# Optimization experiments

Measured on AMD Instinct MI355X. Metric: run time of the kernel, lower is better.

Reference implementation:

```python
import jax, jax.numpy as jnp
import numpy as np

N_NODES = 20000
N_EDGES = 32000
BN_EPS = 1e-5


def _w(key, fan_in, fan_out):
    return jax.random.normal(key, (fan_in, fan_out), jnp.float32) / np.sqrt(fan_in).astype(np.float32)


def setup_inputs() -> dict:
    key = jax.random.key(0)
    ks = jax.random.split(key, 16)
    x = jax.random.normal(ks[0], (N_NODES, 5120), jnp.float32)
    edge_index = jax.random.randint(ks[1], (2, N_EDGES), 0, N_NODES, dtype=jnp.int64)
    return dict(
        x=x,
        W1l=_w(ks[2], 5120, 1680), b1=jnp.zeros((1680,), jnp.float32), W1r=_w(ks[3], 5120, 1680),
        W2l=_w(ks[4], 1680, 640), b2=jnp.zeros((640,), jnp.float32), W2r=_w(ks[5], 1680, 640),
        bn_gamma=jax.random.uniform(ks[6], (1680,), jnp.float32, 0.5, 1.5),
        bn_beta=jax.random.normal(ks[7], (1680,), jnp.float32) * 0.1,
        bn_mean=jnp.zeros((1680,), jnp.float32),
        bn_var=jnp.ones((1680,), jnp.float32),
        lin1_W=_w(ks[8], 640, 320), lin1_b=jnp.zeros((320,), jnp.float32),
        lin2_W=_w(ks[9], 320, 160), lin2_b=jnp.zeros((160,), jnp.float32),
        lin3_W=_w(ks[10], 160, 2), lin3_b=jnp.zeros((2,), jnp.float32),
        edge_index=edge_index,
    )


def _segment_mean(feat, dst, n):
    # mean-aggregate messages feat[e] into their destination node; 0 for isolated nodes (PyG semantics)
    s = jax.ops.segment_sum(feat, dst, num_segments=n)
    cnt = jax.ops.segment_sum(jnp.ones((dst.shape[0],), feat.dtype), dst, num_segments=n)
    return s / jnp.maximum(cnt, 1.0)[:, None]


def reference(x, W1l, b1, W1r, W2l, b2, W2r, bn_gamma, bn_beta, bn_mean, bn_var,
              lin1_W, lin1_b, lin2_W, lin2_b, lin3_W, lin3_b, edge_index):
    src, dst = edge_index[0], edge_index[1]
    n = x.shape[0]
    # SAGEConv 1: lin_l(mean_j x_j) + lin_r(x_i)
    h = _segment_mean(x[src], dst, n) @ W1l + b1 + x @ W1r
    h = jax.nn.relu(h)
    # BatchNorm1d in eval mode (running stats); dropout inactive in eval
    h = (h - bn_mean) * jax.lax.rsqrt(bn_var + BN_EPS) * bn_gamma + bn_beta
    # SAGEConv 2
    h2 = _segment_mean(h[src], dst, n) @ W2l + b2 + h @ W2r
    o = jax.nn.relu(h2)
    o = jax.nn.relu(o @ lin1_W + lin1_b)
    o = jax.nn.relu(o @ lin2_W + lin2_b)
    return o @ lin3_W + lin3_b
```

## Files before the change

### kernel.cpp

```cpp
#include <hip/hip_runtime.h>
#include <stdint.h>

#define NN 20000
#define NE 32000
#define BN_EPS 1e-5f

typedef __attribute__((ext_vector_type(8))) __bf16 bf16x8;
typedef __attribute__((ext_vector_type(4))) float f32x4;
typedef unsigned short u16;
typedef uint32_t u32;

__device__ __forceinline__ u16 f2bf(float f) {
    u32 u = __float_as_uint(f);
    u += 0x7FFFu + ((u >> 16) & 1u);
    return (u16)(u >> 16);
}
__device__ __forceinline__ float bf2f(u16 u) {
    return __uint_as_float(((u32)u) << 16);
}

__device__ __forceinline__ void gload_lds16(const void* g, void* l) {
    __builtin_amdgcn_global_load_lds(
        (const __attribute__((address_space(1))) void*)g,
        (__attribute__((address_space(3))) void*)(uintptr_t)l,
        16, 0, 0);
}

#define LDSRD(base, r, cb) (*(const bf16x8*)((const char*)(base) + (r)*128 + (cb)))

#define DS_A(apb, qm) do { \
  _Pragma("unroll") for (int m4_ = 0; m4_ < 4; ++m4_) { \
    int r_ = (qm)*128 + m4_*32 + wr16 + lrow; \
    aR[m4_][0] = LDSRD(apb, r_, cb0); \
    aR[m4_][1] = LDSRD(apb, r_, cb1); \
  } } while (0)

#define DS_B(bpb, qn) do { \
  _Pragma("unroll") for (int n2_ = 0; n2_ < 2; ++n2_) { \
    int n_ = (qn)*2 + n2_; \
    int r_ = n_*64 + wc16 + lrow; \
    bR[n_][0] = LDSRD(bpb, r_, cb0); \
    bR[n_][1] = LDSRD(bpb, r_, cb1); \
  } } while (0)

#define MM(qm, qn) do { \
  _Pragma("unroll") for (int m4_ = 0; m4_ < 4; ++m4_) \
  _Pragma("unroll") for (int n2_ = 0; n2_ < 2; ++n2_) { \
    int mi_ = (qm)*4 + m4_, ni_ = (qn)*2 + n2_; \
    acc[mi_][ni_] = __builtin_amdgcn_mfma_f32_16x16x32_bf16(aR[m4_][0], bR[ni_][0], acc[mi_][ni_], 0, 0, 0); \
    acc[mi_][ni_] = __builtin_amdgcn_mfma_f32_16x16x32_bf16(aR[m4_][1], bR[ni_][1], acc[mi_][ni_], 0, 0, 0); \
  } } while (0)

#define PHASE_TOP() do { __builtin_amdgcn_s_barrier(); \
  asm volatile("s_waitcnt lgkmcnt(0)" ::: "memory"); \
  __builtin_amdgcn_s_setprio(1); } while (0)
#define PHASE_END() do { __builtin_amdgcn_s_setprio(0); \
  __builtin_amdgcn_s_barrier(); } while (0)
#define PHASE_END_VM() do { __builtin_amdgcn_s_setprio(0); \
  asm volatile("s_waitcnt vmcnt(6)" ::: "memory"); \
  __builtin_amdgcn_s_barrier(); } while (0)

#define KLOOP_BODY(nit_) do { \
  for (int it = 0; it < (nit_); ++it) { \
    const int t1 = 2 * it + 1, t2 = 2 * it + 2, t3 = 2 * it + 3; \
    DS_A(&As[0][0][0], 0); DS_B(&Bs[0][0][0], 0); \
    SA(1, 1, t1); \
    PHASE_TOP(); MM(0, 0); PHASE_END(); \
    DS_B(&Bs[0][0][0], 1); \
    SA(0, 0, t2); \
    PHASE_TOP(); MM(0, 1); PHASE_END(); \
    DS_A(&As[0][0][0], 1); \
    SB(0, 0, t2); \
    PHASE_TOP(); MM(1, 1); PHASE_END(); \
    SB(0, 1, t2); \
    __builtin_amdgcn_s_barrier(); \
    __builtin_amdgcn_s_setprio(1); \
    MM(1, 0); \
    PHASE_END_VM(); \
    DS_A(&As[1][0][0], 0); DS_B(&Bs[1][0][0], 0); \
    SA(0, 1, t2); \
    PHASE_TOP(); MM(0, 0); PHASE_END(); \
    DS_B(&Bs[1][0][0], 1); \
    SA(1, 0, t3); \
    PHASE_TOP(); MM(0, 1); PHASE_END(); \
    DS_A(&As[1][0][0], 1); \
    SB(1, 0, t3); \
    PHASE_TOP(); MM(1, 1); PHASE_END(); \
    SB(1, 1, t3); \
    __builtin_amdgcn_s_barrier(); \
    __builtin_amdgcn_s_setprio(1); \
    MM(1, 0); \
    PHASE_END_VM(); \
  } } while (0)

__global__ __launch_bounds__(512, 2) void gemm1f(
    const u16* __restrict__ xbf, const u16* __restrict__ w1T,
    u16* __restrict__ y1l, u16* __restrict__ y1r,
    const int* __restrict__ clist, const int* __restrict__ nsrcp)
{
    __shared__ __align__(16) u16 As[2][256][64];
    __shared__ __align__(16) u16 Bs[2][256][64];
    const int K = 5120, lda = 5120;
    const int Km64 = K - 64;

    const int nsrc = nsrcp[0];
    const int nmt_l = (nsrc + 255) >> 8;
    const int nl = nmt_l * 7;
    const int nwg = nl + 553;

    int bid = blockIdx.x;
    if (bid >= nwg) return;
    int q8 = nwg >> 3, r8 = nwg & 7;
    int xcd = bid & 7, lid = bid >> 3;
    int wgid = (xcd < r8 ? xcd * (q8 + 1) : r8 * (q8 + 1) + (xcd - r8) * q8) + lid;

    int roleL = (wgid < nl);
    int local, nmt;
    if (roleL) { local = wgid; nmt = nmt_l; }
    else       { local = wgid - nl; nmt = 79; }
    int g = local / 112;
    int first = g << 4;
    int gsz = nmt - first; gsz = gsz < 16 ? gsz : 16;
    int rem = local - g * 112;
    int mt = first + rem % gsz;
    int nt = rem / gsz;

    const int m0 = mt << 8, n0 = nt << 8;
    const int tid = threadIdx.x;
    const int wid = tid >> 6, ln = tid & 63;
    const int wr = wid >> 2, wc = wid & 3;
    const int lrow = ln & 15, khi = ln >> 4;
    const int wr16 = wr << 4, wc16 = wc << 4;
    const int cb0 = (khi << 4) ^ ((lrow & 7) << 4);
    const int cb1 = cb0 ^ 64;
    const int row0 = tid >> 3;
    const int kel = ((tid & 7) ^ (row0 & 7)) << 3;
    const int dstoff = (tid & 448) << 4;

    const u16* Bp = w1T + (roleL ? (size_t)0 : (size_t)1680 * 5120);
    const u16* aB[4];
    const u16* bB[4];
#pragma unroll
    for (int i = 0; i < 4; ++i) {
        int r = m0 + ((i >> 1) << 7) + ((i & 1) << 6) + row0;
        int ga;
        if (roleL) { int idx = r < nsrc ? r : nsrc - 1; ga = clist[idx]; }
        else       { ga = r < NN ? r : NN - 1; }
        aB[i] = xbf + (size_t)ga * lda + kel;
        int rb = n0 + ((i >> 1) << 7) + ((i & 1) << 6) + row0;
        rb = rb < 1680 ? rb : 1679;
        bB[i] = Bp + (size_t)rb * lda + kel;
    }

#define SA(b, ha, t) do { int ks_ = (t) * 64; if (ks_ > Km64) ks_ = Km64; \
  char* d_ = (char*)&As[b][(ha)*128][0] + dstoff; \
  gload_lds16(aB[(ha)*2] + ks_, d_); \
  gload_lds16(aB[(ha)*2 + 1] + ks_, d_ + 8192); } while (0)
#define SB(b, hb, t) do { int ks_ = (t) * 64; if (ks_ > Km64) ks_ = Km64; \
  char* d_ = (char*)&Bs[b][(hb)*128][0] + dstoff; \
  gload_lds16(bB[(hb)*2] + ks_, d_); \
  gload_lds16(bB[(hb)*2 + 1] + ks_, d_ + 8192); } while (0)

    f32x4 acc[8][4];
#pragma unroll
    for (int m = 0; m < 8; ++m)
#pragma unroll
        for (int n = 0; n < 4; ++n)
#pragma unroll
            for (int j = 0; j < 4; ++j) acc[m][n][j] = 0.f;
    bf16x8 aR[4][2], bR[4][2];

    SA(0, 0, 0); SB(0, 0, 0); SB(0, 1, 0); SA(0, 1, 0);
    SA(1, 0, 1); SB(1, 0, 1); SB(1, 1, 1);
    asm volatile("s_waitcnt vmcnt(6)" ::: "memory");
    __builtin_amdgcn_s_barrier();

    KLOOP_BODY(40);

#undef SA
#undef SB

    const int Meff = roleL ? nsrc : NN;
    u16* C = roleL ? y1l : y1r;
#pragma unroll
    for (int m = 0; m < 8; ++m) {
        int gr0 = m0 + m * 32 + wr16 + (khi << 2);
#pragma unroll
        for (int n = 0; n < 4; ++n) {
            int gc = n0 + n * 64 + wc16 + lrow;
            if (gc >= 1680) continue;
#pragma unroll
            for (int j = 0; j < 4; ++j) {
                int gr = gr0 + j;
                if (gr >= Meff) continue;
                C[(size_t)gr * 1680 + gc] = f2bf(acc[m][n][j]);
            }
        }
    }
}

__global__ __launch_bounds__(512, 2) void gemm256(
    const u16* __restrict__ A, const u16* __restrict__ B, u16* __restrict__ C,
    int M, int N, int K, int lda, int ldb, int ldc)
{
    __shared__ __align__(16) u16 As[2][256][64];
    __shared__ __align__(16) u16 Bs[2][256][64];

    const int nmt = (M + 255) >> 8;
    const int ntn = (N + 255) >> 8;
    const int nwg = nmt * ntn;

    int bid = blockIdx.x;
    int q8 = nwg >> 3, r8 = nwg & 7;
    int xcd = bid & 7, lid = bid >> 3;
    int wgid = (xcd < r8 ? xcd * (q8 + 1) : r8 * (q8 + 1) + (xcd - r8) * q8) + lid;
    int per = ntn << 3;
    int g = wgid / per;
    int first = g << 3;
    int gsz = nmt - first; gsz = gsz < 8 ? gsz : 8;
    int rem = wgid - g * per;
    int mt = first + rem % gsz;
    int nt = rem / gsz;

    const int m0 = mt << 8, n0 = nt << 8;
    const int tid = threadIdx.x;
    const int wid = tid >> 6, ln = tid & 63;
    const int wr = wid >> 2, wc = wid & 3;
    const int lrow = ln & 15, khi = ln >> 4;
    const int wr16 = wr << 4, wc16 = wc << 4;
    const int cb0 = (khi << 4) ^ ((lrow & 7) << 4);
    const int cb1 = cb0 ^ 64;
    const int row0 = tid >> 3;
    const int kel = ((tid & 7) ^ (row0 & 7)) << 3;
    const int dstoff = (tid & 448) << 4;
    const int Km64 = K - 64;

#define SA(b, ha, t) do { int ks_ = (t) * 64; if (ks_ > Km64) ks_ = Km64; \
  int ra_ = m0 + (ha)*128 + row0;      ra_ = ra_ < M ? ra_ : M - 1; \
  int rb_ = m0 + (ha)*128 + row0 + 64; rb_ = rb_ < M ? rb_ : M - 1; \
  char* d_ = (char*)&As[b][(ha)*128][0] + dstoff; \
  gload_lds16(A + (size_t)ra_ * lda + ks_ + kel, d_); \
  gload_lds16(A + (size_t)rb_ * lda + ks_ + kel, d_ + 8192); } while (0)
#define SB(b, hb, t) do { int ks_ = (t) * 64; if (ks_ > Km64) ks_ = Km64; \
  int ra_ = n0 + (hb)*128 + row0;      ra_ = ra_ < N ? ra_ : N - 1; \
  int rb_ = n0 + (hb)*128 + row0 + 64; rb_ = rb_ < N ? rb_ : N - 1; \
  char* d_ = (char*)&Bs[b][(hb)*128][0] + dstoff; \
  gload_lds16(B + (size_t)ra_ * ldb + ks_ + kel, d_); \
  gload_lds16(B + (size_t)rb_ * ldb + ks_ + kel, d_ + 8192); } while (0)

    f32x4 acc[8][4];
#pragma unroll
    for (int m = 0; m < 8; ++m)
#pragma unroll
        for (int n = 0; n < 4; ++n)
#pragma unroll
            for (int j = 0; j < 4; ++j) acc[m][n][j] = 0.f;
    bf16x8 aR[4][2], bR[4][2];

    SA(0, 0, 0); SB(0, 0, 0); SB(0, 1, 0); SA(0, 1, 0);
    SA(1, 0, 1); SB(1, 0, 1); SB(1, 1, 1);
    asm volatile("s_waitcnt vmcnt(6)" ::: "memory");
    __builtin_amdgcn_s_barrier();

    const int nit = K >> 7;
    KLOOP_BODY(nit);

#undef SA
#undef SB

#pragma unroll
    for (int m = 0; m < 8; ++m) {
        int gr0 = m0 + m * 32 + wr16 + (khi << 2);
#pragma unroll
        for (int n = 0; n < 4; ++n) {
            int gc = n0 + n * 64 + wc16 + lrow;
            if (gc >= N) continue;
#pragma unroll
            for (int j = 0; j < 4; ++j) {
                int gr = gr0 + j;
                if (gr >= M) continue;
                C[(size_t)gr * ldc + gc] = f2bf(acc[m][n][j]);
            }
        }
    }
}

template <int EPI>
__global__ __launch_bounds__(256, 2) void gemm_bt(
    const u16* __restrict__ A, const u16* __restrict__ B, u16* __restrict__ C,
    const float* __restrict__ bias, int M, int N, int K, int lda, int ldb, int ldc)
{
    __shared__ __align__(16) u16 As[128][64];
    __shared__ __align__(16) u16 Bs[128][64];

    const int nmt = (M + 127) >> 7;
    const int ntn = (N + 127) >> 7;
    int bid = blockIdx.x;
    int per_grp = 16 * ntn;
    int g = bid / per_grp;
    int first = g * 16;
    int gsz = min(16, nmt - first);
    int rem = bid - g * per_grp;
    int mt = first + rem % gsz;
    int nt = rem / gsz;

    const int m0 = mt << 7, n0 = nt << 7;
    const int tid = threadIdx.x;
    const int wv = tid >> 6, ln = tid & 63;
    const int wr = wv >> 1, wc = wv & 1;

    f32x4 acc[4][4];
#pragma unroll
    for (int m = 0; m < 4; ++m)
#pragma unroll
        for (int n = 0; n < 4; ++n)
#pragma unroll
            for (int j = 0; j < 4; ++j) acc[m][n][j] = 0.f;

    const int lrow = ln & 15;
    const int koff = (ln >> 4) << 3;

    for (int k0 = 0; k0 < K; k0 += 64) {
#pragma unroll
        for (int r = 0; r < 4; ++r) {
            int c = r * 256 + wv * 64 + ln;
            int row = c >> 3;
            int kc = (c & 7) << 3;
            int ga = m0 + row; ga = ga < M ? ga : M - 1;
            gload_lds16(A + (size_t)ga * lda + (k0 + kc),
                        (char*)&As[0][0] + (size_t)(r * 256 + wv * 64) * 16);
            int gb = n0 + row; gb = gb < N ? gb : N - 1;
            gload_lds16(B + (size_t)gb * ldb + (k0 + kc),
                        (char*)&Bs[0][0] + (size_t)(r * 256 + wv * 64) * 16);
        }
        __syncthreads();
#pragma unroll
        for (int kk = 0; kk < 2; ++kk) {
            bf16x8 af[4], bfr[4];
            const int krd = (kk << 5) + koff;
#pragma unroll
            for (int m = 0; m < 4; ++m)
                af[m] = *(const bf16x8*)&As[(wr << 6) + (m << 4) + lrow][krd];
#pragma unroll
            for (int n = 0; n < 4; ++n)
                bfr[n] = *(const bf16x8*)&Bs[(wc << 6) + (n << 4) + lrow][krd];
#pragma unroll
            for (int m = 0; m < 4; ++m)
#pragma unroll
                for (int n = 0; n < 4; ++n)
                    acc[m][n] = __builtin_amdgcn_mfma_f32_16x16x32_bf16(
                        af[m], bfr[n], acc[m][n], 0, 0, 0);
        }
        __syncthreads();
    }

    const int colb = ln & 15;
    const int rowb = (ln >> 4) << 2;
#pragma unroll
    for (int m = 0; m < 4; ++m) {
        int gr0 = m0 + (wr << 6) + (m << 4) + rowb;
#pragma unroll
        for (int n = 0; n < 4; ++n) {
            int gc = n0 + (wc << 6) + (n << 4) + colb;
            if (gc >= N) continue;
            float bv = (EPI == 1) ? bias[gc] : 0.f;
#pragma unroll
            for (int j = 0; j < 4; ++j) {
                int gr = gr0 + j;
                if (gr >= M) continue;
                float v = acc[m][n][j];
                if (EPI == 1) { v += bv; v = v > 0.f ? v : 0.f; }
                C[(size_t)gr * ldc + gc] = f2bf(v);
            }
        }
    }
}

__global__ void cvt_bf16(const float* __restrict__ in, u16* __restrict__ out, int n4)
{
    for (int i = blockIdx.x * 256 + threadIdx.x; i < n4; i += gridDim.x * 256) {
        float4 v = ((const float4*)in)[i];
        ushort4 o;
        o.x = f2bf(v.x); o.y = f2bf(v.y); o.z = f2bf(v.z); o.w = f2bf(v.w);
        ((ushort4*)out)[i] = o;
    }
}

__global__ void wtrans(const float* __restrict__ s0, const float* __restrict__ s1,
                       u16* __restrict__ out, int Kin, int Kpad, int N, int nsplit)
{
    __shared__ float t[32][33];
    int k0 = blockIdx.x << 5, n0 = blockIdx.y << 5;
    int tx = threadIdx.x, ty = threadIdx.y;
#pragma unroll
    for (int i = 0; i < 4; ++i) {
        int k = k0 + ty + (i << 3);
        int n = n0 + tx;
        float v = 0.f;
        if (k < Kin && n < N)
            v = (n < nsplit) ? s0[(size_t)k * nsplit + n]
                             : s1[(size_t)k * (N - nsplit) + (n - nsplit)];
        t[ty + (i << 3)][tx] = v;
    }
    __syncthreads();
#pragma unroll
    for (int i = 0; i < 4; ++i) {
        int n = n0 + ty + (i << 3);
        int k = k0 + tx;
        if (n < N && k < Kpad)
            out[(size_t)n * Kpad + k] = f2bf(t[tx][ty + (i << 3)]);
    }
}

__global__ void deg_mark_k(const int* __restrict__ src, const int* __restrict__ dst,
                           int* __restrict__ deg, int* __restrict__ cmark, int ne)
{
    int e = blockIdx.x * 256 + threadIdx.x;
    if (e < ne) {
        atomicAdd(&deg[dst[e]], 1);
        cmark[src[e]] = 1;
    }
}

__global__ __launch_bounds__(256) void scan2_k(
    const int* __restrict__ deg, int* __restrict__ off, int* __restrict__ cur,
    int* __restrict__ cmark, int* __restrict__ clist, int* __restrict__ nsrcp)
{
    __shared__ int part[256];
    int t = threadIdx.x;
    int st = t * 79;
    int s = 0;
    for (int j = 0; j < 79; ++j) { int i = st + j; if (i < NN) s += deg[i]; }
    part[t] = s;
    __syncthreads();
    for (int d = 1; d < 256; d <<= 1) {
        int v = (t >= d) ? part[t - d] : 0;
        __syncthreads(); part[t] += v; __syncthreads();
    }
    int run = part[t] - s;
    for (int j = 0; j < 79; ++j) {
        int i = st + j;
        if (i < NN) { off[i] = run; cur[i] = run; run += deg[i]; }
    }
    if (t == 255) off[NN] = NE;
    __syncthreads();
    int s2 = 0;
    for (int j = 0; j < 79; ++j) { int i = st + j; if (i < NN) s2 += cmark[i]; }
    part[t] = s2;
    __syncthreads();
    for (int d = 1; d < 256; d <<= 1) {
        int v = (t >= d) ? part[t - d] : 0;
        __syncthreads(); part[t] += v; __syncthreads();
    }
    int run2 = part[t] - s2;
    for (int j = 0; j < 79; ++j) {
        int i = st + j;
        if (i < NN) {
            int m = cmark[i];
            if (m) clist[run2] = i;
            cmark[i] = run2;
            run2 += m;
        }
    }
    if (t == 255) nsrcp[0] = part[255];
}

__global__ void fill_k(const int* __restrict__ src, const int* __restrict__ dst,
                       int* __restrict__ cur, const int* __restrict__ cidx,
                       int* __restrict__ esrc, int ne)
{
    int e = blockIdx.x * 256 + threadIdx.x;
    if (e < ne) {
        int p = atomicAdd(&cur[dst[e]], 1);
        esrc[p] = cidx[src[e]];
    }
}

__global__ __launch_bounds__(256) void agg_bn_k(
    const u16* __restrict__ y1l, const u16* __restrict__ y1r,
    const int* __restrict__ off, const int* __restrict__ esrc,
    const float* __restrict__ b1, const float* __restrict__ gam, const float* __restrict__ bet,
    const float* __restrict__ mn, const float* __restrict__ vr, u16* __restrict__ h)
{
    int b = blockIdx.x, t = threadIdx.x;
    int o0 = off[b], o1 = off[b + 1];
    int deg = o1 - o0;
    int col = t << 3;
    if (t >= 210) {
        if (t < 224) {
            bf16x8 z = (bf16x8)(__bf16)0.f;
            *(bf16x8*)&h[(size_t)b * 1792 + col] = z;
        }
        return;
    }
    float s[8];
#pragma unroll
    for (int i = 0; i < 8; ++i) s[i] = 0.f;
    for (int j = o0; j < o1; ++j) {
        int sc = esrc[j];
        bf16x8 v = *(const bf16x8*)&y1l[(size_t)sc * 1680 + col];
#pragma unroll
        for (int i = 0; i < 8; ++i) s[i] += (float)v[i];
    }
    float inv = 1.f / (deg > 1 ? (float)deg : 1.f);
    bf16x8 yr = *(const bf16x8*)&y1r[(size_t)b * 1680 + col];
    float4 bb0 = *(const float4*)&b1[col],  bb1 = *(const float4*)&b1[col + 4];
    float4 g0  = *(const float4*)&gam[col], g1  = *(const float4*)&gam[col + 4];
    float4 be0 = *(const float4*)&bet[col], be1 = *(const float4*)&bet[col + 4];
    float4 m0  = *(const float4*)&mn[col],  m1  = *(const float4*)&mn[col + 4];
    float4 v0  = *(const float4*)&vr[col],  v1  = *(const float4*)&vr[col + 4];
    float bbv[8] = {bb0.x, bb0.y, bb0.z, bb0.w, bb1.x, bb1.y, bb1.z, bb1.w};
    float gv[8]  = {g0.x,  g0.y,  g0.z,  g0.w,  g1.x,  g1.y,  g1.z,  g1.w};
    float bev[8] = {be0.x, be0.y, be0.z, be0.w, be1.x, be1.y, be1.z, be1.w};
    float mv[8]  = {m0.x,  m0.y,  m0.z,  m0.w,  m1.x,  m1.y,  m1.z,  m1.w};
    float vv[8]  = {v0.x,  v0.y,  v0.z,  v0.w,  v1.x,  v1.y,  v1.z,  v1.w};
    u16 o[8];
#pragma unroll
    for (int i = 0; i < 8; ++i) {
        float tv = fmaxf(s[i] * inv + bbv[i] + (float)yr[i], 0.f);
        tv = (tv - mv[i]) * rsqrtf(vv[i] + BN_EPS) * gv[i] + bev[i];
        o[i] = f2bf(tv);
    }
    *(ushort4*)&h[(size_t)b * 1792 + col]     = *(ushort4*)&o[0];
    *(ushort4*)&h[(size_t)b * 1792 + col + 4] = *(ushort4*)&o[4];
}

__global__ __launch_bounds__(192) void agg_h2_k(
    const u16* __restrict__ y2, const int* __restrict__ off, const int* __restrict__ esrc,
    const int* __restrict__ clist, const int* __restrict__ nsrcp,
    const float* __restrict__ b2, u16* __restrict__ h2)
{
    int b = blockIdx.x, t = threadIdx.x;
    if (t >= 160) return;
    int o0 = off[b], o1 = off[b + 1];
    int deg = o1 - o0;
    float sx = 0.f, sy = 0.f, sz = 0.f, sw = 0.f;
    for (int j = o0; j < o1; ++j) {
        int s = clist[esrc[j]];
        ushort4 v = *(const ushort4*)&y2[(size_t)s * 1280 + (t << 2)];
        sx += bf2f(v.x); sy += bf2f(v.y); sz += bf2f(v.z); sw += bf2f(v.w);
    }
    float inv = 1.f / (deg > 1 ? (float)deg : 1.f);
    int col = t << 2;
    ushort4 yr = *(const ushort4*)&y2[(size_t)b * 1280 + 640 + col];
    float4 bb = *(const float4*)&b2[col];
    ushort4 o;
    o.x = f2bf(fmaxf(sx * inv + bb.x + bf2f(yr.x), 0.f));
    o.y = f2bf(fmaxf(sy * inv + bb.y + bf2f(yr.y), 0.f));
    o.z = f2bf(fmaxf(sz * inv + bb.z + bf2f(yr.z), 0.f));
    o.w = f2bf(fmaxf(sw * inv + bb.w + bf2f(yr.w), 0.f));
    *(ushort4*)&h2[(size_t)b * 640 + col] = o;
}

__global__ void lin3_k(const u16* __restrict__ o2, const float* __restrict__ W,
                       const float* __restrict__ b, float* __restrict__ out)
{
    __shared__ float ws[320];
    for (int j = threadIdx.x; j < 320; j += 256) ws[j] = W[j];
    __syncthreads();
    int i = blockIdx.x * 256 + threadIdx.x;
    if (i >= NN) return;
    float a0 = b[0], a1 = b[1];
    const u16* row = o2 + (size_t)i * 160;
#pragma unroll
    for (int k8 = 0; k8 < 20; ++k8) {
        ushort4 v0 = *(const ushort4*)&row[k8 * 8];
        ushort4 v1 = *(const ushort4*)&row[k8 * 8 + 4];
        int kb = k8 * 8;
        float f;
        f = bf2f(v0.x); a0 += f * ws[(kb + 0) * 2]; a1 += f * ws[(kb + 0) * 2 + 1];
        f = bf2f(v0.y); a0 += f * ws[(kb + 1) * 2]; a1 += f * ws[(kb + 1) * 2 + 1];
        f = bf2f(v0.z); a0 += f * ws[(kb + 2) * 2]; a1 += f * ws[(kb + 2) * 2 + 1];
        f = bf2f(v0.w); a0 += f * ws[(kb + 3) * 2]; a1 += f * ws[(kb + 3) * 2 + 1];
        f = bf2f(v1.x); a0 += f * ws[(kb + 4) * 2]; a1 += f * ws[(kb + 4) * 2 + 1];
        f = bf2f(v1.y); a0 += f * ws[(kb + 5) * 2]; a1 += f * ws[(kb + 5) * 2 + 1];
        f = bf2f(v1.z); a0 += f * ws[(kb + 6) * 2]; a1 += f * ws[(kb + 6) * 2 + 1];
        f = bf2f(v1.w); a0 += f * ws[(kb + 7) * 2]; a1 += f * ws[(kb + 7) * 2 + 1];
    }
    out[(size_t)i * 2 + 0] = a0;
    out[(size_t)i * 2 + 1] = a1;
}

extern "C" void kernel_launch(void* const* d_in, const int* in_sizes, int n_in,
                              void* d_out, int out_size, void* d_ws, size_t ws_size,
                              hipStream_t stream)
{
    const float* x     = (const float*)d_in[0];
    const float* W1l   = (const float*)d_in[1];
    const float* b1    = (const float*)d_in[2];
    const float* W1r   = (const float*)d_in[3];
    const float* W2l   = (const float*)d_in[4];
    const float* b2    = (const float*)d_in[5];
    const float* W2r   = (const float*)d_in[6];
    const float* gam   = (const float*)d_in[7];
    const float* bet   = (const float*)d_in[8];
    const float* bmean = (const float*)d_in[9];
    const float* bvar  = (const float*)d_in[10];
    const float* l1W   = (const float*)d_in[11];
    const float* l1b   = (const float*)d_in[12];
    const float* l2W   = (const float*)d_in[13];
    const float* l2b   = (const float*)d_in[14];
    const float* l3W   = (const float*)d_in[15];
    const float* l3b   = (const float*)d_in[16];
    const int*   ei    = (const int*)d_in[17];
    const int* src = ei, * dst = ei + NE;

    char* ws = (char*)d_ws;
    u16*   y1l  = (u16*)(ws + 0);
    u16*   y1r  = (u16*)(ws + 68000000);
    u16*   y2   = (u16*)(ws + 0);
    u16*   o1   = (u16*)(ws + 0);
    u16*   o2   = (u16*)(ws + 16000000);
    u16*   xbf  = (u16*)(ws + 136000000);
    u16*   hbuf = (u16*)(ws + 136000000);
    u16*   h2   = (u16*)(ws + 136000000);
    u16*   w1T  = (u16*)(ws + 341000000);
    u16*   w2T  = (u16*)(ws + 341000000);
    u16*   l1T  = (u16*)(ws + 346000000);
    u16*   l2T  = (u16*)(ws + 347000000);
    int*   deg   = (int*)(ws + 375500000);
    int*   off   = (int*)(ws + 375584000);
    int*   cur   = (int*)(ws + 375668000);
    int*   cmark = (int*)(ws + 375752000);
    int*   clist = (int*)(ws + 375836000);
    int*   esrc  = (int*)(ws + 375920000);
    int*   nsrcp = (int*)(ws + 376050000);

    hipMemsetAsync(deg, 0, NN * sizeof(int), stream);
    hipMemsetAsync(cmark, 0, NN * sizeof(int), stream);
    deg_mark_k<<<(NE + 255) / 256, 256, 0, stream>>>(src, dst, deg, cmark, NE);
    scan2_k<<<1, 256, 0, stream>>>(deg, off, cur, cmark, clist, nsrcp);
    fill_k<<<(NE + 255) / 256, 256, 0, stream>>>(src, dst, cur, cmark, esrc, NE);

    cvt_bf16<<<2048, 256, 0, stream>>>(x, xbf, NN * 5120 / 4);
    wtrans<<<dim3(160, 105), dim3(32, 8), 0, stream>>>(W1l, W1r, w1T, 5120, 5120, 3360, 1680);

    gemm1f<<<1106, 512, 0, stream>>>(xbf, w1T, y1l, y1r, clist, nsrcp);

    agg_bn_k<<<NN, 256, 0, stream>>>(y1l, y1r, off, esrc, b1, gam, bet, bmean, bvar, hbuf);

    wtrans<<<dim3(56, 40), dim3(32, 8), 0, stream>>>(W2l, W2r, w2T, 1680, 1792, 1280, 640);

    gemm256<<<79 * 5, 512, 0, stream>>>(hbuf, w2T, y2, NN, 1280, 1792, 1792, 1792, 1280);

    agg_h2_k<<<NN, 192, 0, stream>>>(y2, off, esrc, clist, nsrcp, b2, h2);

    wtrans<<<dim3(20, 10), dim3(32, 8), 0, stream>>>(l1W, l1W, l1T, 640, 640, 320, 320);
    wtrans<<<dim3(10, 5), dim3(32, 8), 0, stream>>>(l2W, l2W, l2T, 320, 320, 160, 160);

    gemm_bt<1><<<157 * 3, 256, 0, stream>>>(h2, l1T, o1, l1b,
                                            NN, 320, 640, 640, 640, 320);

    gemm_bt<1><<<157 * 2, 256, 0, stream>>>(o1, l2T, o2, l2b,
                                            NN, 160, 320, 320, 320, 160);

    lin3_k<<<(NN + 255) / 256, 256, 0, stream>>>(o2, l3W, l3b, (float*)d_out);
}
```

Measured before the change: 1.073 ms.

## Fuse MLP head into one kernel, merge weight transposes and memsets, retile gemm1 groups

Replaces the two gemm_bt launches and lin3_k with a single mlp_head_k that keeps each 64-row tile's intermediates in LDS through all three linear layers. This removes the o1/o2 global round trips and two kernel launches. The W1, lin1 and lin2 transposes are merged into one launch, and the two memsets become one by placing cmark next to deg. The gemm1f M-tile grouping also shrinks from 16 to 8 rows of tiles, which changes L2 reuse. The fused head reads B fragments straight from global memory without LDS staging and runs only 313 blocks, which may underuse the device.

```diff
diff --git a/kernel.cpp b/kernel.cpp
--- a/kernel.cpp
+++ b/kernel.cpp
@@ -118,10 +118,10 @@
     int local, nmt;
     if (roleL) { local = wgid; nmt = nmt_l; }
     else       { local = wgid - nl; nmt = 79; }
-    int g = local / 112;
-    int first = g << 4;
-    int gsz = nmt - first; gsz = gsz < 16 ? gsz : 16;
-    int rem = local - g * 112;
+    int g = local / 56;
+    int first = g << 3;
+    int gsz = nmt - first; gsz = gsz < 8 ? gsz : 8;
+    int rem = local - g * 56;
     int mt = first + rem % gsz;
     int nt = rem / gsz;
 
@@ -285,97 +285,6 @@
     }
 }
 
-template <int EPI>
-__global__ __launch_bounds__(256, 2) void gemm_bt(
-    const u16* __restrict__ A, const u16* __restrict__ B, u16* __restrict__ C,
-    const float* __restrict__ bias, int M, int N, int K, int lda, int ldb, int ldc)
-{
-    __shared__ __align__(16) u16 As[128][64];
-    __shared__ __align__(16) u16 Bs[128][64];
-
-    const int nmt = (M + 127) >> 7;
-    const int ntn = (N + 127) >> 7;
-    int bid = blockIdx.x;
-    int per_grp = 16 * ntn;
-    int g = bid / per_grp;
-    int first = g * 16;
-    int gsz = min(16, nmt - first);
-    int rem = bid - g * per_grp;
-    int mt = first + rem % gsz;
-    int nt = rem / gsz;
-
-    const int m0 = mt << 7, n0 = nt << 7;
-    const int tid = threadIdx.x;
-    const int wv = tid >> 6, ln = tid & 63;
-    const int wr = wv >> 1, wc = wv & 1;
-
-    f32x4 acc[4][4];
-#pragma unroll
-    for (int m = 0; m < 4; ++m)
-#pragma unroll
-        for (int n = 0; n < 4; ++n)
-#pragma unroll
-            for (int j = 0; j < 4; ++j) acc[m][n][j] = 0.f;
-
-    const int lrow = ln & 15;
-    const int koff = (ln >> 4) << 3;
-
-    for (int k0 = 0; k0 < K; k0 += 64) {
-#pragma unroll
-        for (int r = 0; r < 4; ++r) {
-            int c = r * 256 + wv * 64 + ln;
-            int row = c >> 3;
-            int kc = (c & 7) << 3;
-            int ga = m0 + row; ga = ga < M ? ga : M - 1;
-            gload_lds16(A + (size_t)ga * lda + (k0 + kc),
-                        (char*)&As[0][0] + (size_t)(r * 256 + wv * 64) * 16);
-            int gb = n0 + row; gb = gb < N ? gb : N - 1;
-            gload_lds16(B + (size_t)gb * ldb + (k0 + kc),
-                        (char*)&Bs[0][0] + (size_t)(r * 256 + wv * 64) * 16);
-        }
-        __syncthreads();
-#pragma unroll
-        for (int kk = 0; kk < 2; ++kk) {
-            bf16x8 af[4], bfr[4];
-            const int krd = (kk << 5) + koff;
-#pragma unroll
-            for (int m = 0; m < 4; ++m)
-                af[m] = *(const bf16x8*)&As[(wr << 6) + (m << 4) + lrow][krd];
-#pragma unroll
-            for (int n = 0; n < 4; ++n)
-                bfr[n] = *(const bf16x8*)&Bs[(wc << 6) + (n << 4) + lrow][krd];
-#pragma unroll
-            for (int m = 0; m < 4; ++m)
-#pragma unroll
-                for (int n = 0; n < 4; ++n)
-                    acc[m][n] = __builtin_amdgcn_mfma_f32_16x16x32_bf16(
-                        af[m], bfr[n], acc[m][n], 0, 0, 0);
-        }
-        __syncthreads();
-    }
-
-    const int colb = ln & 15;
-    const int rowb = (ln >> 4) << 2;
-#pragma unroll
-    for (int m = 0; m < 4; ++m) {
-        int gr0 = m0 + (wr << 6) + (m << 4) + rowb;
-#pragma unroll
-        for (int n = 0; n < 4; ++n) {
-            int gc = n0 + (wc << 6) + (n << 4) + colb;
-            if (gc >= N) continue;
-            float bv = (EPI == 1) ? bias[gc] : 0.f;
-#pragma unroll
-            for (int j = 0; j < 4; ++j) {
-                int gr = gr0 + j;
-                if (gr >= M) continue;
-                float v = acc[m][n][j];
-                if (EPI == 1) { v += bv; v = v > 0.f ? v : 0.f; }
-                C[(size_t)gr * ldc + gc] = f2bf(v);
-            }
-        }
-    }
-}
-
 __global__ void cvt_bf16(const float* __restrict__ in, u16* __restrict__ out, int n4)
 {
     for (int i = blockIdx.x * 256 + threadIdx.x; i < n4; i += gridDim.x * 256) {
@@ -386,11 +295,12 @@
     }
 }
 
-__global__ void wtrans(const float* __restrict__ s0, const float* __restrict__ s1,
-                       u16* __restrict__ out, int Kin, int Kpad, int N, int nsplit)
+__device__ __forceinline__ void wtrans_body(
+    const float* __restrict__ s0, const float* __restrict__ s1,
+    u16* __restrict__ out, int Kin, int Kpad, int N, int nsplit, int kx, int ny)
 {
     __shared__ float t[32][33];
-    int k0 = blockIdx.x << 5, n0 = blockIdx.y << 5;
+    int k0 = kx << 5, n0 = ny << 5;
     int tx = threadIdx.x, ty = threadIdx.y;
 #pragma unroll
     for (int i = 0; i < 4; ++i) {
@@ -410,6 +320,28 @@
         if (n < N && k < Kpad)
             out[(size_t)n * Kpad + k] = f2bf(t[tx][ty + (i << 3)]);
     }
+}
+
+__global__ void wtrans_all(const float* __restrict__ W1l, const float* __restrict__ W1r,
+                           const float* __restrict__ l1W, const float* __restrict__ l2W,
+                           u16* __restrict__ w1T, u16* __restrict__ l1T, u16* __restrict__ l2T)
+{
+    int b = blockIdx.x;
+    if (b < 16800)
+        wtrans_body(W1l, W1r, w1T, 5120, 5120, 3360, 1680, b % 160, b / 160);
+    else if (b < 17000) {
+        b -= 16800;
+        wtrans_body(l1W, l1W, l1T, 640, 640, 320, 320, b % 20, b / 20);
+    } else {
+        b -= 17000;
+        wtrans_body(l2W, l2W, l2T, 320, 320, 160, 160, b % 10, b / 10);
+    }
+}
+
+__global__ void wtrans_w2(const float* __restrict__ W2l, const float* __restrict__ W2r,
+                          u16* __restrict__ w2T)
+{
+    wtrans_body(W2l, W2r, w2T, 1680, 1792, 1280, 640, blockIdx.x, blockIdx.y);
 }
 
 __global__ void deg_mark_k(const int* __restrict__ src, const int* __restrict__ dst,
@@ -527,7 +459,7 @@
 
 __global__ __launch_bounds__(192) void agg_h2_k(
     const u16* __restrict__ y2, const int* __restrict__ off, const int* __restrict__ esrc,
-    const int* __restrict__ clist, const int* __restrict__ nsrcp,
+    const int* __restrict__ clist,
     const float* __restrict__ b2, u16* __restrict__ h2)
 {
     int b = blockIdx.x, t = threadIdx.x;
@@ -552,33 +484,124 @@
     *(ushort4*)&h2[(size_t)b * 640 + col] = o;
 }
 
-__global__ void lin3_k(const u16* __restrict__ o2, const float* __restrict__ W,
-                       const float* __restrict__ b, float* __restrict__ out)
-{
-    __shared__ float ws[320];
-    for (int j = threadIdx.x; j < 320; j += 256) ws[j] = W[j];
+__global__ __launch_bounds__(256) void mlp_head_k(
+    const u16* __restrict__ h2, const u16* __restrict__ l1T, const float* __restrict__ l1b,
+    const u16* __restrict__ l2T, const float* __restrict__ l2b,
+    const float* __restrict__ l3W, const float* __restrict__ l3b, float* __restrict__ out)
+{
+    __shared__ __align__(16) u16 h2s[64][648];
+    __shared__ __align__(16) u16 o1s[64][328];
+    __shared__ __align__(16) u16 o2s[64][168];
+    __shared__ float l3s[320];
+
+    const int tid = threadIdx.x;
+    const int r0 = blockIdx.x * 64;
+    const int wv = tid >> 6, ln = tid & 63;
+    const int lrow = ln & 15, khi = ln >> 4;
+
+    for (int j = tid; j < 320; j += 256) l3s[j] = l3W[j];
+    for (int c = tid; c < 64 * 80; c += 256) {
+        int row = c / 80, c8 = c - row * 80;
+        int gr = r0 + row; gr = gr < NN ? gr : NN - 1;
+        bf16x8 v = *(const bf16x8*)&h2[(size_t)gr * 640 + c8 * 8];
+        *(bf16x8*)&h2s[row][c8 * 8] = v;
+    }
     __syncthreads();
-    int i = blockIdx.x * 256 + threadIdx.x;
-    if (i >= NN) return;
-    float a0 = b[0], a1 = b[1];
-    const u16* row = o2 + (size_t)i * 160;
-#pragma unroll
-    for (int k8 = 0; k8 < 20; ++k8) {
-        ushort4 v0 = *(const ushort4*)&row[k8 * 8];
-        ushort4 v1 = *(const ushort4*)&row[k8 * 8 + 4];
-        int kb = k8 * 8;
-        float f;
-        f = bf2f(v0.x); a0 += f * ws[(kb + 0) * 2]; a1 += f * ws[(kb + 0) * 2 + 1];
-        f = bf2f(v0.y); a0 += f * ws[(kb + 1) * 2]; a1 += f * ws[(kb + 1) * 2 + 1];
-        f = bf2f(v0.z); a0 += f * ws[(kb + 2) * 2]; a1 += f * ws[(kb + 2) * 2 + 1];
-        f = bf2f(v0.w); a0 += f * ws[(kb + 3) * 2]; a1 += f * ws[(kb + 3) * 2 + 1];
-        f = bf2f(v1.x); a0 += f * ws[(kb + 4) * 2]; a1 += f * ws[(kb + 4) * 2 + 1];
-        f = bf2f(v1.y); a0 += f * ws[(kb + 5) * 2]; a1 += f * ws[(kb + 5) * 2 + 1];
-        f = bf2f(v1.z); a0 += f * ws[(kb + 6) * 2]; a1 += f * ws[(kb + 6) * 2 + 1];
-        f = bf2f(v1.w); a0 += f * ws[(kb + 7) * 2]; a1 += f * ws[(kb + 7) * 2 + 1];
-    }
-    out[(size_t)i * 2 + 0] = a0;
-    out[(size_t)i * 2 + 1] = a1;
+
+    {
+        f32x4 a1[4][5];
+#pragma unroll
+        for (int m = 0; m < 4; ++m)
+#pragma unroll
+            for (int n = 0; n < 5; ++n)
+#pragma unroll
+                for (int j = 0; j < 4; ++j) a1[m][n][j] = 0.f;
+        const u16* bp[5];
+#pragma unroll
+        for (int n = 0; n < 5; ++n)
+            bp[n] = l1T + (size_t)(wv * 80 + n * 16 + lrow) * 640 + khi * 8;
+        bf16x8 bcur[5], bnxt[5];
+#pragma unroll
+        for (int n = 0; n < 5; ++n) bcur[n] = *(const bf16x8*)(bp[n]);
+        for (int ks = 0; ks < 20; ++ks) {
+            if (ks < 19) {
+#pragma unroll
+                for (int n = 0; n < 5; ++n)
+                    bnxt[n] = *(const bf16x8*)(bp[n] + (ks + 1) * 32);
+            }
+            bf16x8 a[4];
+            int kb = ks * 32 + khi * 8;
+#pragma unroll
+            for (int m = 0; m < 4; ++m)
+                a[m] = *(const bf16x8*)&h2s[m * 16 + lrow][kb];
+#pragma unroll
+            for (int m = 0; m < 4; ++m)
+#pragma unroll
+                for (int n = 0; n < 5; ++n)
+                    a1[m][n] = __builtin_amdgcn_mfma_f32_16x16x32_bf16(a[m], bcur[n], a1[m][n], 0, 0, 0);
+#pragma unroll
+            for (int n = 0; n < 5; ++n) bcur[n] = bnxt[n];
+        }
+#pragma unroll
+        for (int n = 0; n < 5; ++n) {
+            int col = wv * 80 + n * 16 + lrow;
+            float bb = l1b[col];
+#pragma unroll
+            for (int m = 0; m < 4; ++m) {
+                int rw = m * 16 + khi * 4;
+#pragma unroll
+                for (int j = 0; j < 4; ++j)
+                    o1s[rw + j][col] = f2bf(fmaxf(a1[m][n][j] + bb, 0.f));
+            }
+        }
+    }
+    __syncthreads();
+
+    {
+        f32x4 a2[10];
+#pragma unroll
+        for (int n = 0; n < 10; ++n)
+#pragma unroll
+            for (int j = 0; j < 4; ++j) a2[n][j] = 0.f;
+        for (int ks = 0; ks < 10; ++ks) {
+            int kb = ks * 32 + khi * 8;
+            bf16x8 a = *(const bf16x8*)&o1s[wv * 16 + lrow][kb];
+#pragma unroll
+            for (int n = 0; n < 10; ++n) {
+                bf16x8 b = *(const bf16x8*)&l2T[(size_t)(n * 16 + lrow) * 320 + kb];
+                a2[n] = __builtin_amdgcn_mfma_f32_16x16x32_bf16(a, b, a2[n], 0, 0, 0);
+            }
+        }
+#pragma unroll
+        for (int n = 0; n < 10; ++n) {
+            int col = n * 16 + lrow;
+            float bb = l2b[col];
+            int rw = wv * 16 + khi * 4;
+#pragma unroll
+            for (int j = 0; j < 4; ++j)
+                o2s[rw + j][col] = f2bf(fmaxf(a2[n][j] + bb, 0.f));
+        }
+    }
+    __syncthreads();
+
+    if (tid < 64) {
+        int gr = r0 + tid;
+        if (gr < NN) {
+            float a0 = l3b[0], a1v = l3b[1];
+#pragma unroll
+            for (int c8 = 0; c8 < 20; ++c8) {
+                bf16x8 v = *(const bf16x8*)&o2s[tid][c8 * 8];
+#pragma unroll
+                for (int i = 0; i < 8; ++i) {
+                    float f = (float)v[i];
+                    a0  += f * l3s[(c8 * 8 + i) * 2];
+                    a1v += f * l3s[(c8 * 8 + i) * 2 + 1];
+                }
+            }
+            out[(size_t)gr * 2 + 0] = a0;
+            out[(size_t)gr * 2 + 1] = a1v;
+        }
+    }
 }
 
 extern "C" void kernel_launch(void* const* d_in, const int* in_sizes, int n_in,
@@ -609,50 +632,38 @@
     u16*   y1l  = (u16*)(ws + 0);
     u16*   y1r  = (u16*)(ws + 68000000);
     u16*   y2   = (u16*)(ws + 0);
-    u16*   o1   = (u16*)(ws + 0);
-    u16*   o2   = (u16*)(ws + 16000000);
+    u16*   l1T  = (u16*)(ws + 135200000);
+    u16*   l2T  = (u16*)(ws + 135700000);
     u16*   xbf  = (u16*)(ws + 136000000);
     u16*   hbuf = (u16*)(ws + 136000000);
     u16*   h2   = (u16*)(ws + 136000000);
     u16*   w1T  = (u16*)(ws + 341000000);
     u16*   w2T  = (u16*)(ws + 341000000);
-    u16*   l1T  = (u16*)(ws + 346000000);
-    u16*   l2T  = (u16*)(ws + 347000000);
     int*   deg   = (int*)(ws + 375500000);
-    int*   off   = (int*)(ws + 375584000);
-    int*   cur   = (int*)(ws + 375668000);
-    int*   cmark = (int*)(ws + 375752000);
-    int*   clist = (int*)(ws + 375836000);
-    int*   esrc  = (int*)(ws + 375920000);
-    int*   nsrcp = (int*)(ws + 376050000);
-
-    hipMemsetAsync(deg, 0, NN * sizeof(int), stream);
-    hipMemsetAsync(cmark, 0, NN * sizeof(int), stream);
+    int*   cmark = (int*)(ws + 375580000);
+    int*   off   = (int*)(ws + 375660000);
+    int*   cur   = (int*)(ws + 375740008);
+    int*   clist = (int*)(ws + 375820008);
+    int*   esrc  = (int*)(ws + 375900008);
+    int*   nsrcp = (int*)(ws + 376028008);
+
+    hipMemsetAsync(deg, 0, 2 * NN * sizeof(int), stream);
     deg_mark_k<<<(NE + 255) / 256, 256, 0, stream>>>(src, dst, deg, cmark, NE);
     scan2_k<<<1, 256, 0, stream>>>(deg, off, cur, cmark, clist, nsrcp);
     fill_k<<<(NE + 255) / 256, 256, 0, stream>>>(src, dst, cur, cmark, esrc, NE);
 
     cvt_bf16<<<2048, 256, 0, stream>>>(x, xbf, NN * 5120 / 4);
-    wtrans<<<dim3(160, 105), dim3(32, 8), 0, stream>>>(W1l, W1r, w1T, 5120, 5120, 3360, 1680);
+    wtrans_all<<<17050, dim3(32, 8), 0, stream>>>(W1l, W1r, l1W, l2W, w1T, l1T, l2T);
 
     gemm1f<<<1106, 512, 0, stream>>>(xbf, w1T, y1l, y1r, clist, nsrcp);
 
     agg_bn_k<<<NN, 256, 0, stream>>>(y1l, y1r, off, esrc, b1, gam, bet, bmean, bvar, hbuf);
 
-    wtrans<<<dim3(56, 40), dim3(32, 8), 0, stream>>>(W2l, W2r, w2T, 1680, 1792, 1280, 640);
+    wtrans_w2<<<dim3(56, 40), dim3(32, 8), 0, stream>>>(W2l, W2r, w2T);
 
     gemm256<<<79 * 5, 512, 0, stream>>>(hbuf, w2T, y2, NN, 1280, 1792, 1792, 1792, 1280);
 
-    agg_h2_k<<<NN, 192, 0, stream>>>(y2, off, esrc, clist, nsrcp, b2, h2);
-
-    wtrans<<<dim3(20, 10), dim3(32, 8), 0, stream>>>(l1W, l1W, l1T, 640, 640, 320, 320);
-    wtrans<<<dim3(10, 5), dim3(32, 8), 0, stream>>>(l2W, l2W, l2T, 320, 320, 160, 160);
-
-    gemm_bt<1><<<157 * 3, 256, 0, stream>>>(h2, l1T, o1, l1b,
-                                            NN, 320, 640, 640, 640, 320);
-
-    gemm_bt<1><<<157 * 2, 256, 0, stream>>>(o1, l2T, o2, l2b,
-                                            NN, 160, 320, 320, 320, 160);
-
-    lin3_k<<<(NN + 255) / 256, 256, 0, stream>>>(o2, l3W, l3b, (float*)d_out);
-}
+    agg_h2_k<<<NN, 192, 0, stream>>>(y2, off, esrc, clist, b2, h2);
+
+    mlp_head_k<<<313, 256, 0, stream>>>(h2, l1T, l1b, l2T, l2b, l3W, l3b, (float*)d_out);
+}
```

New measurement: 1.063 ms. No clear change (-0.9%).
